# Kernel optimization log

Hardware: AMD Instinct MI355X
Metric: run time of the kernel (lower is better)

The kernel has to match this reference:

```python
import jax, jax.numpy as jnp
import numpy as np

H = 1024; NH = 16; HD = H // NH  # hidden, heads, head_dim

def setup_inputs() -> dict:
    key = jax.random.key(0)
    ks = jax.random.split(key, 9)
    s = 1.0 / np.sqrt(H)
    return {
        "hidden_states": jax.random.normal(ks[0], (2, 2048, H), jnp.float32),
        "Wq": jax.random.uniform(ks[1], (H, H), jnp.float32, -s, s),
        "bq": jnp.zeros((H,), jnp.float32),
        "Wk": jax.random.uniform(ks[2], (H, H), jnp.float32, -s, s),
        "bk": jnp.zeros((H,), jnp.float32),
        "Wv": jax.random.uniform(ks[3], (H, H), jnp.float32, -s, s),
        "bv": jnp.zeros((H,), jnp.float32),
        "Wo": jax.random.uniform(ks[4], (H, H), jnp.float32, -s, s),
        "bo": jnp.zeros((H,), jnp.float32),
    }

def reference(hidden_states, Wq, bq, Wk, bk, Wv, bv, Wo, bo):
    B, S, _ = hidden_states.shape
    def heads(x):  # [B,S,H] -> [B,NH,S,HD]
        return x.reshape(B, S, NH, HD).transpose(0, 2, 1, 3)
    q = heads(hidden_states @ Wq + bq)
    k = heads(hidden_states @ Wk + bk)
    v = heads(hidden_states @ Wv + bv)
    scores = jnp.einsum('bhqd,bhkd->bhqk', q, k) / jnp.sqrt(jnp.float32(HD))
    causal = jnp.where(jnp.tril(jnp.ones((S, S), bool)), 0.0, -jnp.inf)
    probs = jax.nn.softmax(scores + causal[None, None], axis=-1)
    ctx = jnp.einsum('bhqk,bhkd->bhqd', probs, v)
    ctx = ctx.transpose(0, 2, 1, 3).reshape(B, S, H)
    return ctx @ Wo + bo
```

## Files before the change

kernel.cpp:

```cpp
#include <hip/hip_runtime.h>
#include <hip/hip_bf16.h>

#define BB 2
#define SS 2048
#define HH 1024
#define NHH 16
#define HDD 64
#define MM (BB*SS)
#define QKV_N (3*HH)

typedef _Float16 f16x8 __attribute__((ext_vector_type(8)));
typedef _Float16 f16x4 __attribute__((ext_vector_type(4)));
typedef float f32x4 __attribute__((ext_vector_type(4)));

#define MFMA16(a,b,c) __builtin_amdgcn_mfma_f32_16x16x32_f16((a),(b),(c),0,0,0)

__device__ __forceinline__ void gl2lds16(const _Float16* g, _Float16* l) {
    __builtin_amdgcn_global_load_lds(
        (const __attribute__((address_space(1))) void*)g,
        (__attribute__((address_space(3))) void*)l, 16, 0, 0);
}

__global__ void prep_kernel(const float* __restrict__ X,
                            const float* __restrict__ W0, const float* __restrict__ W1,
                            const float* __restrict__ W2, const float* __restrict__ W3,
                            _Float16* __restrict__ Xh,
                            _Float16* __restrict__ WqkvT, _Float16* __restrict__ WoT) {
    __shared__ float t[32][33];
    int z = blockIdx.z;
    int tx = threadIdx.x, ty = threadIdx.y;
    if (z >= 4) {
        size_t row0 = (size_t)(z - 4) * 1024 + blockIdx.y * 32;
        int col0 = blockIdx.x * 32;
#pragma unroll
        for (int r = ty; r < 32; r += 8) {
            float v = X[(row0 + r) * HH + col0 + tx];
            Xh[(row0 + r) * HH + col0 + tx] = (_Float16)v;
        }
        return;
    }
    const float* src = (z == 0) ? W0 : (z == 1) ? W1 : (z == 2) ? W2 : W3;
    _Float16* dst = (z < 3) ? (WqkvT + (size_t)z * HH * HH) : WoT;
    int k0 = blockIdx.y * 32, n0 = blockIdx.x * 32;
#pragma unroll
    for (int r = ty; r < 32; r += 8)
        t[r][tx] = src[(size_t)(k0 + r) * HH + (n0 + tx)];
    __syncthreads();
#pragma unroll
    for (int r = ty; r < 32; r += 8)
        dst[(size_t)(n0 + r) * HH + (k0 + tx)] = (_Float16)t[tx][r];
}

template<int MODE>
__global__ __launch_bounds__(256) void gemm128_kernel(
    const _Float16* __restrict__ A, const _Float16* __restrict__ Bt,
    const float* __restrict__ bias0, const float* __restrict__ bias1, const float* __restrict__ bias2,
    _Float16* __restrict__ Qh, _Float16* __restrict__ Kh, _Float16* __restrict__ Vt,
    float* __restrict__ Out)
{
    const int K = HH;
    const int NT = K / 32;
    __shared__ _Float16 smem[16896];

    int row0 = blockIdx.y * 128, n0 = blockIdx.x * 128;
    int tid = threadIdx.x;
    int w = tid >> 6, l = tid & 63, m16 = l & 15, quad = l >> 4;
    int wm = w >> 1, wn = w & 1;

    int srow = w * 32 + (l >> 2);
    int sch = (l & 3) ^ ((l >> 2) & 3) ^ ((l >> 4) & 3);
    const _Float16* aptr = A + (size_t)(row0 + srow) * K + sch * 8;
    const _Float16* bptr = Bt + (size_t)(n0 + srow) * K + sch * 8;

    int gsw = (m16 & 3) ^ ((m16 >> 2) & 3);
    int acol = (quad ^ gsw) * 8;

    f32x4 zero4 = {0.f, 0.f, 0.f, 0.f};
    f32x4 acc[4][4];
#pragma unroll
    for (int i = 0; i < 4; ++i)
#pragma unroll
        for (int j = 0; j < 4; ++j) acc[i][j] = zero4;

    auto stage = [&](int t, int buf) {
        int k0 = t * 32;
        int ao = buf * 4096 + (w * 32) * 32;
        int bo = 8192 + buf * 4096 + (w * 32) * 32;
        gl2lds16(aptr + k0, smem + ao);
        gl2lds16(aptr + (size_t)16 * K + k0, smem + ao + 16 * 32);
        gl2lds16(bptr + k0, smem + bo);
        gl2lds16(bptr + (size_t)16 * K + k0, smem + bo + 16 * 32);
    };

    stage(0, 0);
    for (int t = 0; t < NT; ++t) {
        int cur = t & 1;
        asm volatile("s_waitcnt vmcnt(0)" ::: "memory");
        __syncthreads();
        if (t + 1 < NT) stage(t + 1, cur ^ 1);
        const _Float16* Asr = smem + cur * 4096;
        const _Float16* Bsr = smem + 8192 + cur * 4096;
        f16x8 af[4], bf[4];
#pragma unroll
        for (int i = 0; i < 4; ++i)
            af[i] = *(const f16x8*)&Asr[(wm * 64 + i * 16 + m16) * 32 + acol];
#pragma unroll
        for (int j = 0; j < 4; ++j)
            bf[j] = *(const f16x8*)&Bsr[(wn * 64 + j * 16 + m16) * 32 + acol];
#pragma unroll
        for (int i = 0; i < 4; ++i)
#pragma unroll
            for (int j = 0; j < 4; ++j)
                acc[i][j] = MFMA16(af[i], bf[j], acc[i][j]);
    }

    if (MODE == 1) {
#pragma unroll
        for (int j = 0; j < 4; ++j) {
            int n = n0 + wn * 64 + j * 16 + m16;
            float bi = bias0[n];
#pragma unroll
            for (int i = 0; i < 4; ++i)
#pragma unroll
                for (int r = 0; r < 4; ++r) {
                    int mg = row0 + wm * 64 + i * 16 + quad * 4 + r;
                    Out[(size_t)mg * HH + n] = acc[i][j][r] + bi;
                }
        }
        return;
    }

    int which = n0 >> 10;
    const float* bias = (which == 0) ? bias0 : (which == 1) ? bias1 : bias2;
    __syncthreads();
#pragma unroll
    for (int j = 0; j < 4; ++j) {
        int n_local = wn * 64 + j * 16 + m16;
        float bi = bias[(n0 + n_local) & 1023];
#pragma unroll
        for (int i = 0; i < 4; ++i)
#pragma unroll
            for (int r = 0; r < 4; ++r) {
                int m_local = wm * 64 + i * 16 + quad * 4 + r;
                float v = acc[i][j][r] + bi;
                if (which == 0) v *= 0.18033688011112042f;
                if (which == 2) smem[n_local * 132 + m_local] = (_Float16)v;
                else            smem[m_local * 132 + n_local] = (_Float16)v;
            }
    }
    __syncthreads();

    int b = row0 >> 11, s0 = row0 & 2047;
    if (which == 2) {
#pragma unroll
        for (int p = 0; p < 8; ++p) {
            int n_local = p * 16 + (tid >> 4);
            int schunk = tid & 15;
            f16x8 v = *(const f16x8*)&smem[n_local * 132 + schunk * 8];
            int nw = (n0 + n_local) & 1023;
            int hh = nw >> 6, d = nw & 63;
            *(f16x8*)&Vt[((size_t)(b * NHH + hh) * HDD + d) * SS + s0 + schunk * 8] = v;
        }
    } else {
        _Float16* dst = (which == 0) ? Qh : Kh;
        int hh0 = (n0 & 1023) >> 6;
#pragma unroll
        for (int p = 0; p < 8; ++p) {
            int m_local = p * 16 + (tid >> 4);
            int seg = tid & 15;
            f16x8 v = *(const f16x8*)&smem[m_local * 132 + seg * 8];
            int hh = hh0 + (seg >> 3), d = (seg & 7) * 8;
            *(f16x8*)&dst[((size_t)(b * NHH + hh) * SS + s0 + m_local) * HDD + d] = v;
        }
    }
}

typedef _Float16 PlRow[72];

__device__ __forceinline__ void attn_body(
    int kt, int qbase, int m16, int quad,
    const f16x8& aq0, const f16x8& aq1,
    const f16x8 bk[4][2], const f16x8 bv[4][2],
    f32x4 o[4], float* lsum, PlRow* Pl)
{
    f32x4 zero4 = {0.f, 0.f, 0.f, 0.f};
    f32x4 sc[4];
#pragma unroll
    for (int s = 0; s < 4; ++s) {
        sc[s] = MFMA16(aq0, bk[s][0], zero4);
        sc[s] = MFMA16(aq1, bk[s][1], sc[s]);
    }
#pragma unroll
    for (int s = 0; s < 4; ++s) {
        int key = kt + s * 16 + m16;
#pragma unroll
        for (int r = 0; r < 4; ++r) {
            int qrow = qbase + quad * 4 + r;
            float p = (key > qrow) ? 0.0f : exp2f(sc[s][r]);
            lsum[r] += p;
            Pl[quad * 4 + r][s * 16 + m16] = (_Float16)p;
        }
    }
    asm volatile("s_waitcnt lgkmcnt(0)" ::: "memory");
    f16x8 pf0 = *(const f16x8*)&Pl[m16][quad * 8];
    f16x8 pf1 = *(const f16x8*)&Pl[m16][32 + quad * 8];
#pragma unroll
    for (int c = 0; c < 4; ++c) {
        o[c] = MFMA16(pf0, bv[c][0], o[c]);
        o[c] = MFMA16(pf1, bv[c][1], o[c]);
    }
}

__global__ __launch_bounds__(256, 2) void attn_kernel(
    const _Float16* __restrict__ Qh, const _Float16* __restrict__ Kh,
    const _Float16* __restrict__ Vt, _Float16* __restrict__ Ctx)
{
    __shared__ _Float16 Kb[64 * 64];
    __shared__ _Float16 Vb[64 * 64];
    __shared__ _Float16 Pl[4][16][72];

    int tid = threadIdx.x;
    int w = tid >> 6, l = tid & 63;
    int m16 = l & 15, quad = l >> 4;
    int b = blockIdx.z, h = blockIdx.y;
    int tA = blockIdx.x, tB = 31 - tA;

    const _Float16* Q = Qh + (size_t)(b * NHH + h) * SS * HDD;
    const _Float16* K = Kh + (size_t)(b * NHH + h) * SS * HDD;
    const _Float16* V = Vt + (size_t)(b * NHH + h) * HDD * SS;

    int qbA = tA * 64 + w * 16, qbB = tB * 64 + w * 16;
    f16x8 aqA0 = *(const f16x8*)(Q + (size_t)(qbA + m16) * HDD + quad * 8);
    f16x8 aqA1 = *(const f16x8*)(Q + (size_t)(qbA + m16) * HDD + 32 + quad * 8);
    f16x8 aqB0 = *(const f16x8*)(Q + (size_t)(qbB + m16) * HDD + quad * 8);
    f16x8 aqB1 = *(const f16x8*)(Q + (size_t)(qbB + m16) * HDD + 32 + quad * 8);

    int srow = w * 16 + (l >> 3);
    int sch = (l & 7) ^ (l >> 3);
    const _Float16* kg = K + (size_t)srow * HDD + sch * 8;
    const _Float16* vg = V + (size_t)srow * SS + sch * 8;
    _Float16* kl0 = &Kb[(w * 16) * 64];
    _Float16* kl1 = &Kb[(w * 16 + 8) * 64];
    _Float16* vl0 = &Vb[(w * 16) * 64];
    _Float16* vl1 = &Vb[(w * 16 + 8) * 64];

    int swz = m16 & 7;
    int cka = (quad ^ swz) * 8;
    int ckb = ((quad + 4) ^ swz) * 8;

    f32x4 zero4 = {0.f, 0.f, 0.f, 0.f};
    f32x4 oA[4], oB[4];
#pragma unroll
    for (int c = 0; c < 4; ++c) { oA[c] = zero4; oB[c] = zero4; }
    float lsA[4] = {0.f, 0.f, 0.f, 0.f}, lsB[4] = {0.f, 0.f, 0.f, 0.f};

    for (int t = 0; t <= tB; ++t) {
        int kt = t * 64;
        gl2lds16(kg + (size_t)kt * HDD, kl0);
        gl2lds16(kg + (size_t)(kt + 8) * HDD, kl1);
        gl2lds16(vg + kt, vl0);
        gl2lds16(vg + (size_t)8 * SS + kt, vl1);
        asm volatile("s_waitcnt vmcnt(0)" ::: "memory");
        __syncthreads();

        f16x8 bk[4][2], bv[4][2];
#pragma unroll
        for (int s = 0; s < 4; ++s) {
            const _Float16* kr = &Kb[(s * 16 + m16) * 64];
            bk[s][0] = *(const f16x8*)(kr + cka);
            bk[s][1] = *(const f16x8*)(kr + ckb);
        }
#pragma unroll
        for (int c = 0; c < 4; ++c) {
            const _Float16* vr = &Vb[(c * 16 + m16) * 64];
            bv[c][0] = *(const f16x8*)(vr + cka);
            bv[c][1] = *(const f16x8*)(vr + ckb);
        }

        attn_body(kt, qbB, m16, quad, aqB0, aqB1, bk, bv, oB, lsB, Pl[w]);
        if (t <= tA)
            attn_body(kt, qbA, m16, quad, aqA0, aqA1, bk, bv, oA, lsA, Pl[w]);
        __syncthreads();
    }

#pragma unroll
    for (int half = 0; half < 2; ++half) {
        f32x4* o = half ? oB : oA;
        float* ls = half ? lsB : lsA;
        int qb = half ? qbB : qbA;
#pragma unroll
        for (int r = 0; r < 4; ++r) {
            float rs = ls[r];
#pragma unroll
            for (int off = 1; off < 16; off <<= 1) rs += __shfl_xor(rs, off);
            float inv = 1.0f / rs;
            size_t rowoff = ((size_t)(b * SS) + qb + quad * 4 + r) * HH + h * HDD;
#pragma unroll
            for (int c = 0; c < 4; ++c)
                Ctx[rowoff + c * 16 + m16] = (_Float16)(o[c][r] * inv);
        }
    }
}

extern "C" void kernel_launch(void* const* d_in, const int* in_sizes, int n_in,
                              void* d_out, int out_size, void* d_ws, size_t ws_size,
                              hipStream_t stream) {
    const float* hs = (const float*)d_in[0];
    const float* Wq = (const float*)d_in[1];
    const float* bq = (const float*)d_in[2];
    const float* Wk = (const float*)d_in[3];
    const float* bk = (const float*)d_in[4];
    const float* Wv = (const float*)d_in[5];
    const float* bv = (const float*)d_in[6];
    const float* Wo = (const float*)d_in[7];
    const float* bo = (const float*)d_in[8];
    float* out = (float*)d_out;

    size_t off = 0;
    auto alloc = [&](size_t bytes) {
        void* p = (char*)d_ws + off;
        off += (bytes + 255) & ~(size_t)255;
        return p;
    };
    _Float16* Xh    = (_Float16*)alloc((size_t)MM * HH * 2);
    _Float16* WqkvT = (_Float16*)alloc((size_t)3 * HH * HH * 2);
    _Float16* WoT   = (_Float16*)alloc((size_t)HH * HH * 2);
    _Float16* Qh    = (_Float16*)alloc((size_t)BB * NHH * SS * HDD * 2);
    _Float16* Kh    = (_Float16*)alloc((size_t)BB * NHH * SS * HDD * 2);
    _Float16* Vt    = (_Float16*)alloc((size_t)BB * NHH * SS * HDD * 2);
    _Float16* Ctx   = (_Float16*)alloc((size_t)MM * HH * 2);

    prep_kernel<<<dim3(32, 32, 8), dim3(32, 8), 0, stream>>>(
        hs, Wq, Wk, Wv, Wo, Xh, WqkvT, WoT);
    gemm128_kernel<0><<<dim3(QKV_N / 128, MM / 128), 256, 0, stream>>>(
        Xh, WqkvT, bq, bk, bv, Qh, Kh, Vt, nullptr);
    attn_kernel<<<dim3(16, NHH, BB), 256, 0, stream>>>(Qh, Kh, Vt, Ctx);
    gemm128_kernel<1><<<dim3(HH / 128, MM / 128), 256, 0, stream>>>(
        Ctx, WoT, bo, bo, bo, nullptr, nullptr, nullptr, out);
}
```

Measured before the change: 208.3 us.

## Double-buffer K/V tiles and interleave both query tiles' attention computation

Adds double-buffered LDS for K and V so the next tile is loaded with global_load_lds while the current tile is computed, and drops the trailing barrier per iteration. It also inlines the two query-tile bodies and interleaves them: both score MFMAs first, then both softmax passes into separate P buffers, then both PV MFMAs. This gives more independent MFMA work between dependencies. LDS use doubles, which may limit occupancy, and the vmcnt(0) wait at the loop top still waits for the prefetch issued one iteration earlier.

```diff
diff --git a/kernel.cpp b/kernel.cpp
--- a/kernel.cpp
+++ b/kernel.cpp
@@ -175,49 +175,13 @@
     }
 }
 
-typedef _Float16 PlRow[72];
-
-__device__ __forceinline__ void attn_body(
-    int kt, int qbase, int m16, int quad,
-    const f16x8& aq0, const f16x8& aq1,
-    const f16x8 bk[4][2], const f16x8 bv[4][2],
-    f32x4 o[4], float* lsum, PlRow* Pl)
-{
-    f32x4 zero4 = {0.f, 0.f, 0.f, 0.f};
-    f32x4 sc[4];
-#pragma unroll
-    for (int s = 0; s < 4; ++s) {
-        sc[s] = MFMA16(aq0, bk[s][0], zero4);
-        sc[s] = MFMA16(aq1, bk[s][1], sc[s]);
-    }
-#pragma unroll
-    for (int s = 0; s < 4; ++s) {
-        int key = kt + s * 16 + m16;
-#pragma unroll
-        for (int r = 0; r < 4; ++r) {
-            int qrow = qbase + quad * 4 + r;
-            float p = (key > qrow) ? 0.0f : exp2f(sc[s][r]);
-            lsum[r] += p;
-            Pl[quad * 4 + r][s * 16 + m16] = (_Float16)p;
-        }
-    }
-    asm volatile("s_waitcnt lgkmcnt(0)" ::: "memory");
-    f16x8 pf0 = *(const f16x8*)&Pl[m16][quad * 8];
-    f16x8 pf1 = *(const f16x8*)&Pl[m16][32 + quad * 8];
-#pragma unroll
-    for (int c = 0; c < 4; ++c) {
-        o[c] = MFMA16(pf0, bv[c][0], o[c]);
-        o[c] = MFMA16(pf1, bv[c][1], o[c]);
-    }
-}
-
 __global__ __launch_bounds__(256, 2) void attn_kernel(
     const _Float16* __restrict__ Qh, const _Float16* __restrict__ Kh,
     const _Float16* __restrict__ Vt, _Float16* __restrict__ Ctx)
 {
-    __shared__ _Float16 Kb[64 * 64];
-    __shared__ _Float16 Vb[64 * 64];
-    __shared__ _Float16 Pl[4][16][72];
+    __shared__ _Float16 Kb[2][64 * 64];
+    __shared__ _Float16 Vb[2][64 * 64];
+    __shared__ _Float16 Pl[4][2][16][72];
 
     int tid = threadIdx.x;
     int w = tid >> 6, l = tid & 63;
@@ -239,10 +203,14 @@
     int sch = (l & 7) ^ (l >> 3);
     const _Float16* kg = K + (size_t)srow * HDD + sch * 8;
     const _Float16* vg = V + (size_t)srow * SS + sch * 8;
-    _Float16* kl0 = &Kb[(w * 16) * 64];
-    _Float16* kl1 = &Kb[(w * 16 + 8) * 64];
-    _Float16* vl0 = &Vb[(w * 16) * 64];
-    _Float16* vl1 = &Vb[(w * 16 + 8) * 64];
+
+    auto stage = [&](int t, int buf) {
+        int kt = t * 64;
+        gl2lds16(kg + (size_t)kt * HDD, &Kb[buf][(w * 16) * 64]);
+        gl2lds16(kg + (size_t)(kt + 8) * HDD, &Kb[buf][(w * 16 + 8) * 64]);
+        gl2lds16(vg + kt, &Vb[buf][(w * 16) * 64]);
+        gl2lds16(vg + (size_t)8 * SS + kt, &Vb[buf][(w * 16 + 8) * 64]);
+    };
 
     int swz = m16 & 7;
     int cka = (quad ^ swz) * 8;
@@ -254,33 +222,85 @@
     for (int c = 0; c < 4; ++c) { oA[c] = zero4; oB[c] = zero4; }
     float lsA[4] = {0.f, 0.f, 0.f, 0.f}, lsB[4] = {0.f, 0.f, 0.f, 0.f};
 
+    stage(0, 0);
     for (int t = 0; t <= tB; ++t) {
+        int cur = t & 1;
         int kt = t * 64;
-        gl2lds16(kg + (size_t)kt * HDD, kl0);
-        gl2lds16(kg + (size_t)(kt + 8) * HDD, kl1);
-        gl2lds16(vg + kt, vl0);
-        gl2lds16(vg + (size_t)8 * SS + kt, vl1);
+        bool doA = (t <= tA);
         asm volatile("s_waitcnt vmcnt(0)" ::: "memory");
         __syncthreads();
+        if (t + 1 <= tB) stage(t + 1, cur ^ 1);
 
         f16x8 bk[4][2], bv[4][2];
 #pragma unroll
         for (int s = 0; s < 4; ++s) {
-            const _Float16* kr = &Kb[(s * 16 + m16) * 64];
+            const _Float16* kr = &Kb[cur][(s * 16 + m16) * 64];
             bk[s][0] = *(const f16x8*)(kr + cka);
             bk[s][1] = *(const f16x8*)(kr + ckb);
         }
 #pragma unroll
         for (int c = 0; c < 4; ++c) {
-            const _Float16* vr = &Vb[(c * 16 + m16) * 64];
+            const _Float16* vr = &Vb[cur][(c * 16 + m16) * 64];
             bv[c][0] = *(const f16x8*)(vr + cka);
             bv[c][1] = *(const f16x8*)(vr + ckb);
         }
 
-        attn_body(kt, qbB, m16, quad, aqB0, aqB1, bk, bv, oB, lsB, Pl[w]);
-        if (t <= tA)
-            attn_body(kt, qbA, m16, quad, aqA0, aqA1, bk, bv, oA, lsA, Pl[w]);
-        __syncthreads();
+        f32x4 scB[4], scA[4];
+#pragma unroll
+        for (int s = 0; s < 4; ++s) {
+            scB[s] = MFMA16(aqB0, bk[s][0], zero4);
+            scB[s] = MFMA16(aqB1, bk[s][1], scB[s]);
+        }
+        if (doA) {
+#pragma unroll
+            for (int s = 0; s < 4; ++s) {
+                scA[s] = MFMA16(aqA0, bk[s][0], zero4);
+                scA[s] = MFMA16(aqA1, bk[s][1], scA[s]);
+            }
+        }
+
+#pragma unroll
+        for (int s = 0; s < 4; ++s) {
+            int key = kt + s * 16 + m16;
+#pragma unroll
+            for (int r = 0; r < 4; ++r) {
+                int qrow = qbB + quad * 4 + r;
+                float p = (key > qrow) ? 0.0f : exp2f(scB[s][r]);
+                lsB[r] += p;
+                Pl[w][0][quad * 4 + r][s * 16 + m16] = (_Float16)p;
+            }
+        }
+        if (doA) {
+#pragma unroll
+            for (int s = 0; s < 4; ++s) {
+                int key = kt + s * 16 + m16;
+#pragma unroll
+                for (int r = 0; r < 4; ++r) {
+                    int qrow = qbA + quad * 4 + r;
+                    float p = (key > qrow) ? 0.0f : exp2f(scA[s][r]);
+                    lsA[r] += p;
+                    Pl[w][1][quad * 4 + r][s * 16 + m16] = (_Float16)p;
+                }
+            }
+        }
+        asm volatile("s_waitcnt lgkmcnt(0)" ::: "memory");
+
+        f16x8 pfB0 = *(const f16x8*)&Pl[w][0][m16][quad * 8];
+        f16x8 pfB1 = *(const f16x8*)&Pl[w][0][m16][32 + quad * 8];
+#pragma unroll
+        for (int c = 0; c < 4; ++c) {
+            oB[c] = MFMA16(pfB0, bv[c][0], oB[c]);
+            oB[c] = MFMA16(pfB1, bv[c][1], oB[c]);
+        }
+        if (doA) {
+            f16x8 pfA0 = *(const f16x8*)&Pl[w][1][m16][quad * 8];
+            f16x8 pfA1 = *(const f16x8*)&Pl[w][1][m16][32 + quad * 8];
+#pragma unroll
+            for (int c = 0; c < 4; ++c) {
+                oA[c] = MFMA16(pfA0, bv[c][0], oA[c]);
+                oA[c] = MFMA16(pfA1, bv[c][1], oA[c]);
+            }
+        }
     }
 
 #pragma unroll
```

Measured after the change: 206.3 us. No clear change (-1.0%).

## Double-buffer attention K/V tiles, one query tile per block, split prep kernel

Applied to the files above, without the earlier changes.

The attention kernel now gives each block a single 64-row query tile instead of a paired early/late tile, so the grid doubles to 32 tiles per head, with the heaviest tiles launched first. K/V tiles are double-buffered in LDS so the next tile's global-to-LDS load is issued before computing the current one, and one barrier per iteration is dropped. Occupancy is raised to 3 blocks per CU. The fused prep kernel is split into a vectorized fp32-to-fp16 cast kernel and a 64x64 vectorized weight transpose, which adds one launch but widens memory accesses. The risk is load imbalance from causal tile sizes and extra LDS pressure.

```diff
diff --git a/kernel.cpp b/kernel.cpp
--- a/kernel.cpp
+++ b/kernel.cpp
@@ -21,34 +21,45 @@
         (__attribute__((address_space(3))) void*)l, 16, 0, 0);
 }
 
-__global__ void prep_kernel(const float* __restrict__ X,
-                            const float* __restrict__ W0, const float* __restrict__ W1,
-                            const float* __restrict__ W2, const float* __restrict__ W3,
-                            _Float16* __restrict__ Xh,
-                            _Float16* __restrict__ WqkvT, _Float16* __restrict__ WoT) {
-    __shared__ float t[32][33];
+__global__ void cast4_kernel(const float* __restrict__ x, _Float16* __restrict__ y, int n4) {
+    int i = blockIdx.x * blockDim.x + threadIdx.x;
+    if (i < n4) {
+        float4 v = ((const float4*)x)[i];
+        f16x4 h = {(_Float16)v.x, (_Float16)v.y, (_Float16)v.z, (_Float16)v.w};
+        ((f16x4*)y)[i] = h;
+    }
+}
+
+__global__ __launch_bounds__(256) void transpose_kernel(
+    const float* __restrict__ W0, const float* __restrict__ W1,
+    const float* __restrict__ W2, const float* __restrict__ W3,
+    _Float16* __restrict__ WqkvT, _Float16* __restrict__ WoT)
+{
+    __shared__ float t[64][65];
     int z = blockIdx.z;
-    int tx = threadIdx.x, ty = threadIdx.y;
-    if (z >= 4) {
-        size_t row0 = (size_t)(z - 4) * 1024 + blockIdx.y * 32;
-        int col0 = blockIdx.x * 32;
-#pragma unroll
-        for (int r = ty; r < 32; r += 8) {
-            float v = X[(row0 + r) * HH + col0 + tx];
-            Xh[(row0 + r) * HH + col0 + tx] = (_Float16)v;
-        }
-        return;
-    }
     const float* src = (z == 0) ? W0 : (z == 1) ? W1 : (z == 2) ? W2 : W3;
     _Float16* dst = (z < 3) ? (WqkvT + (size_t)z * HH * HH) : WoT;
-    int k0 = blockIdx.y * 32, n0 = blockIdx.x * 32;
-#pragma unroll
-    for (int r = ty; r < 32; r += 8)
-        t[r][tx] = src[(size_t)(k0 + r) * HH + (n0 + tx)];
+    int k0 = blockIdx.y * 64, n0 = blockIdx.x * 64;
+    int tid = threadIdx.x;
+
+#pragma unroll
+    for (int p = 0; p < 4; ++p) {
+        int row = p * 16 + (tid >> 4);
+        int col4 = (tid & 15) * 4;
+        float4 v = *(const float4*)&src[(size_t)(k0 + row) * HH + n0 + col4];
+        t[row][col4 + 0] = v.x; t[row][col4 + 1] = v.y;
+        t[row][col4 + 2] = v.z; t[row][col4 + 3] = v.w;
+    }
     __syncthreads();
 #pragma unroll
-    for (int r = ty; r < 32; r += 8)
-        dst[(size_t)(n0 + r) * HH + (k0 + tx)] = (_Float16)t[tx][r];
+    for (int p = 0; p < 2; ++p) {
+        int nc = p * 32 + (tid >> 3);
+        int ch = tid & 7;
+        f16x8 o;
+#pragma unroll
+        for (int j = 0; j < 8; ++j) o[j] = (_Float16)t[ch * 8 + j][nc];
+        *(f16x8*)&dst[(size_t)(n0 + nc) * HH + k0 + ch * 8] = o;
+    }
 }
 
 template<int MODE>
@@ -175,130 +186,112 @@
     }
 }
 
-typedef _Float16 PlRow[72];
-
-__device__ __forceinline__ void attn_body(
-    int kt, int qbase, int m16, int quad,
-    const f16x8& aq0, const f16x8& aq1,
-    const f16x8 bk[4][2], const f16x8 bv[4][2],
-    f32x4 o[4], float* lsum, PlRow* Pl)
-{
-    f32x4 zero4 = {0.f, 0.f, 0.f, 0.f};
-    f32x4 sc[4];
-#pragma unroll
-    for (int s = 0; s < 4; ++s) {
-        sc[s] = MFMA16(aq0, bk[s][0], zero4);
-        sc[s] = MFMA16(aq1, bk[s][1], sc[s]);
-    }
-#pragma unroll
-    for (int s = 0; s < 4; ++s) {
-        int key = kt + s * 16 + m16;
-#pragma unroll
-        for (int r = 0; r < 4; ++r) {
-            int qrow = qbase + quad * 4 + r;
-            float p = (key > qrow) ? 0.0f : exp2f(sc[s][r]);
-            lsum[r] += p;
-            Pl[quad * 4 + r][s * 16 + m16] = (_Float16)p;
-        }
-    }
-    asm volatile("s_waitcnt lgkmcnt(0)" ::: "memory");
-    f16x8 pf0 = *(const f16x8*)&Pl[m16][quad * 8];
-    f16x8 pf1 = *(const f16x8*)&Pl[m16][32 + quad * 8];
-#pragma unroll
-    for (int c = 0; c < 4; ++c) {
-        o[c] = MFMA16(pf0, bv[c][0], o[c]);
-        o[c] = MFMA16(pf1, bv[c][1], o[c]);
-    }
-}
-
-__global__ __launch_bounds__(256, 2) void attn_kernel(
+__global__ __launch_bounds__(256, 3) void attn_kernel(
     const _Float16* __restrict__ Qh, const _Float16* __restrict__ Kh,
     const _Float16* __restrict__ Vt, _Float16* __restrict__ Ctx)
 {
-    __shared__ _Float16 Kb[64 * 64];
-    __shared__ _Float16 Vb[64 * 64];
+    __shared__ _Float16 Kb[2][64 * 64];
+    __shared__ _Float16 Vb[2][64 * 64];
     __shared__ _Float16 Pl[4][16][72];
 
     int tid = threadIdx.x;
     int w = tid >> 6, l = tid & 63;
     int m16 = l & 15, quad = l >> 4;
     int b = blockIdx.z, h = blockIdx.y;
-    int tA = blockIdx.x, tB = 31 - tA;
+    int tq = 31 - blockIdx.x;
 
     const _Float16* Q = Qh + (size_t)(b * NHH + h) * SS * HDD;
     const _Float16* K = Kh + (size_t)(b * NHH + h) * SS * HDD;
     const _Float16* V = Vt + (size_t)(b * NHH + h) * HDD * SS;
 
-    int qbA = tA * 64 + w * 16, qbB = tB * 64 + w * 16;
-    f16x8 aqA0 = *(const f16x8*)(Q + (size_t)(qbA + m16) * HDD + quad * 8);
-    f16x8 aqA1 = *(const f16x8*)(Q + (size_t)(qbA + m16) * HDD + 32 + quad * 8);
-    f16x8 aqB0 = *(const f16x8*)(Q + (size_t)(qbB + m16) * HDD + quad * 8);
-    f16x8 aqB1 = *(const f16x8*)(Q + (size_t)(qbB + m16) * HDD + 32 + quad * 8);
+    int qb = tq * 64 + w * 16;
+    f16x8 aq0 = *(const f16x8*)(Q + (size_t)(qb + m16) * HDD + quad * 8);
+    f16x8 aq1 = *(const f16x8*)(Q + (size_t)(qb + m16) * HDD + 32 + quad * 8);
 
     int srow = w * 16 + (l >> 3);
     int sch = (l & 7) ^ (l >> 3);
     const _Float16* kg = K + (size_t)srow * HDD + sch * 8;
     const _Float16* vg = V + (size_t)srow * SS + sch * 8;
-    _Float16* kl0 = &Kb[(w * 16) * 64];
-    _Float16* kl1 = &Kb[(w * 16 + 8) * 64];
-    _Float16* vl0 = &Vb[(w * 16) * 64];
-    _Float16* vl1 = &Vb[(w * 16 + 8) * 64];
+
+    auto stage = [&](int t, int buf) {
+        int kt = t * 64;
+        gl2lds16(kg + (size_t)kt * HDD, &Kb[buf][(w * 16) * 64]);
+        gl2lds16(kg + (size_t)(kt + 8) * HDD, &Kb[buf][(w * 16 + 8) * 64]);
+        gl2lds16(vg + kt, &Vb[buf][(w * 16) * 64]);
+        gl2lds16(vg + (size_t)8 * SS + kt, &Vb[buf][(w * 16 + 8) * 64]);
+    };
 
     int swz = m16 & 7;
     int cka = (quad ^ swz) * 8;
     int ckb = ((quad + 4) ^ swz) * 8;
 
     f32x4 zero4 = {0.f, 0.f, 0.f, 0.f};
-    f32x4 oA[4], oB[4];
-#pragma unroll
-    for (int c = 0; c < 4; ++c) { oA[c] = zero4; oB[c] = zero4; }
-    float lsA[4] = {0.f, 0.f, 0.f, 0.f}, lsB[4] = {0.f, 0.f, 0.f, 0.f};
-
-    for (int t = 0; t <= tB; ++t) {
+    f32x4 o[4];
+#pragma unroll
+    for (int c = 0; c < 4; ++c) o[c] = zero4;
+    float ls[4] = {0.f, 0.f, 0.f, 0.f};
+
+    stage(0, 0);
+    for (int t = 0; t <= tq; ++t) {
+        int cur = t & 1;
         int kt = t * 64;
-        gl2lds16(kg + (size_t)kt * HDD, kl0);
-        gl2lds16(kg + (size_t)(kt + 8) * HDD, kl1);
-        gl2lds16(vg + kt, vl0);
-        gl2lds16(vg + (size_t)8 * SS + kt, vl1);
         asm volatile("s_waitcnt vmcnt(0)" ::: "memory");
         __syncthreads();
+        if (t < tq) stage(t + 1, cur ^ 1);
 
         f16x8 bk[4][2], bv[4][2];
 #pragma unroll
         for (int s = 0; s < 4; ++s) {
-            const _Float16* kr = &Kb[(s * 16 + m16) * 64];
+            const _Float16* kr = &Kb[cur][(s * 16 + m16) * 64];
             bk[s][0] = *(const f16x8*)(kr + cka);
             bk[s][1] = *(const f16x8*)(kr + ckb);
         }
 #pragma unroll
         for (int c = 0; c < 4; ++c) {
-            const _Float16* vr = &Vb[(c * 16 + m16) * 64];
+            const _Float16* vr = &Vb[cur][(c * 16 + m16) * 64];
             bv[c][0] = *(const f16x8*)(vr + cka);
             bv[c][1] = *(const f16x8*)(vr + ckb);
         }
 
-        attn_body(kt, qbB, m16, quad, aqB0, aqB1, bk, bv, oB, lsB, Pl[w]);
-        if (t <= tA)
-            attn_body(kt, qbA, m16, quad, aqA0, aqA1, bk, bv, oA, lsA, Pl[w]);
-        __syncthreads();
-    }
-
-#pragma unroll
-    for (int half = 0; half < 2; ++half) {
-        f32x4* o = half ? oB : oA;
-        float* ls = half ? lsB : lsA;
-        int qb = half ? qbB : qbA;
-#pragma unroll
-        for (int r = 0; r < 4; ++r) {
-            float rs = ls[r];
-#pragma unroll
-            for (int off = 1; off < 16; off <<= 1) rs += __shfl_xor(rs, off);
-            float inv = 1.0f / rs;
-            size_t rowoff = ((size_t)(b * SS) + qb + quad * 4 + r) * HH + h * HDD;
-#pragma unroll
-            for (int c = 0; c < 4; ++c)
-                Ctx[rowoff + c * 16 + m16] = (_Float16)(o[c][r] * inv);
-        }
+        f32x4 sc[4];
+#pragma unroll
+        for (int s = 0; s < 4; ++s) {
+            sc[s] = MFMA16(aq0, bk[s][0], zero4);
+            sc[s] = MFMA16(aq1, bk[s][1], sc[s]);
+        }
+
+#pragma unroll
+        for (int s = 0; s < 4; ++s) {
+            int key = kt + s * 16 + m16;
+#pragma unroll
+            for (int r = 0; r < 4; ++r) {
+                int qrow = qb + quad * 4 + r;
+                float p = (key > qrow) ? 0.0f : exp2f(sc[s][r]);
+                ls[r] += p;
+                Pl[w][quad * 4 + r][s * 16 + m16] = (_Float16)p;
+            }
+        }
+        asm volatile("s_waitcnt lgkmcnt(0)" ::: "memory");
+
+        f16x8 pf0 = *(const f16x8*)&Pl[w][m16][quad * 8];
+        f16x8 pf1 = *(const f16x8*)&Pl[w][m16][32 + quad * 8];
+#pragma unroll
+        for (int c = 0; c < 4; ++c) {
+            o[c] = MFMA16(pf0, bv[c][0], o[c]);
+            o[c] = MFMA16(pf1, bv[c][1], o[c]);
+        }
+    }
+
+#pragma unroll
+    for (int r = 0; r < 4; ++r) {
+        float rs = ls[r];
+#pragma unroll
+        for (int off = 1; off < 16; off <<= 1) rs += __shfl_xor(rs, off);
+        float inv = 1.0f / rs;
+        size_t rowoff = ((size_t)(b * SS) + qb + quad * 4 + r) * HH + h * HDD;
+#pragma unroll
+        for (int c = 0; c < 4; ++c)
+            Ctx[rowoff + c * 16 + m16] = (_Float16)(o[c][r] * inv);
     }
 }
 
@@ -330,11 +323,11 @@
     _Float16* Vt    = (_Float16*)alloc((size_t)BB * NHH * SS * HDD * 2);
     _Float16* Ctx   = (_Float16*)alloc((size_t)MM * HH * 2);
 
-    prep_kernel<<<dim3(32, 32, 8), dim3(32, 8), 0, stream>>>(
-        hs, Wq, Wk, Wv, Wo, Xh, WqkvT, WoT);
+    cast4_kernel<<<(MM * HH / 4 + 255) / 256, 256, 0, stream>>>(hs, Xh, MM * HH / 4);
+    transpose_kernel<<<dim3(16, 16, 4), 256, 0, stream>>>(Wq, Wk, Wv, Wo, WqkvT, WoT);
     gemm128_kernel<0><<<dim3(QKV_N / 128, MM / 128), 256, 0, stream>>>(
         Xh, WqkvT, bq, bk, bv, Qh, Kh, Vt, nullptr);
-    attn_kernel<<<dim3(16, NHH, BB), 256, 0, stream>>>(Qh, Kh, Vt, Ctx);
+    attn_kernel<<<dim3(32, NHH, BB), 256, 0, stream>>>(Qh, Kh, Vt, Ctx);
     gemm128_kernel<1><<<dim3(HH / 128, MM / 128), 256, 0, stream>>>(
         Ctx, WoT, bo, bo, bo, nullptr, nullptr, nullptr, out);
 }
```

After: 234.9 us. 12.8% more time.
